# Kernel optimization log

Hardware: AMD Instinct MI355X
Metric: run time of the kernel (lower is better)

## Reference

```python
import jax, jax.numpy as jnp
import numpy as np

B, N, G = 16, 6000, 256
T = 200                     # TRAIN_ROIS_PER_IMAGE
RATIO = 0.33                # POSITIVE_ROI_RATIO
POS_NUM = int(T * RATIO)    # 66 positive slots
NEG_SLOTS = T - POS_NUM     # 134 negative slots
BBOX_STD = jnp.asarray([0.1, 0.1, 0.2, 0.2], jnp.float32)
EPS = 1e-8


def _rand_boxes(key, b, n):
    # valid [y1,x1,y2,x2] boxes in [0,1]
    k1, k2 = jax.random.split(key)
    tl = jax.random.uniform(k1, (b, n, 2)) * 0.7
    wh = jax.random.uniform(k2, (b, n, 2)) * 0.25 + 0.02
    return jnp.concatenate([tl, tl + wh], axis=-1).astype(jnp.float32)


def setup_inputs() -> dict:
    key = jax.random.key(0)
    k1, k2, k3, k4, k5 = jax.random.split(key, 5)
    rois = _rand_boxes(k1, B, N)
    rois = rois.at[:, N - 1000:].set(0.0)          # zero padding tail (remove_zero_padding)
    gt_boxes = _rand_boxes(k2, B, G)
    gt_ids = jax.random.randint(k3, (B, G), 1, 81, dtype=jnp.int32)
    gt_ids = gt_ids.at[:, G - 32:G - 16].set(-1)   # crowd boxes (ids < 0)
    gt_ids = gt_ids.at[:, G - 16:].set(0)          # padded gt
    gt_boxes = gt_boxes.at[:, G - 16:].set(0.0)
    pos_score = jax.random.uniform(k4, (B, N), dtype=jnp.float32)
    neg_score = jax.random.uniform(k5, (B, N), dtype=jnp.float32)
    return {"rois": rois, "gt_ids": gt_ids, "gt_boxes": gt_boxes,
            "pos_score": pos_score, "neg_score": neg_score}


def _pairwise_iou(a, b):
    # a:[N,4], b:[G,4] -> [N,G]
    y1 = jnp.maximum(a[:, None, 0], b[None, :, 0])
    x1 = jnp.maximum(a[:, None, 1], b[None, :, 1])
    y2 = jnp.minimum(a[:, None, 2], b[None, :, 2])
    x2 = jnp.minimum(a[:, None, 3], b[None, :, 3])
    inter = jnp.clip(y2 - y1, 0.0) * jnp.clip(x2 - x1, 0.0)
    area_a = (a[:, 2] - a[:, 0]) * (a[:, 3] - a[:, 1])
    area_b = (b[:, 2] - b[:, 0]) * (b[:, 3] - b[:, 1])
    union = area_a[:, None] + area_b[None, :] - inter
    return inter / jnp.maximum(union, EPS)


def _bbox_offset(boxes, gt):
    h = jnp.maximum(boxes[:, 2] - boxes[:, 0], EPS)
    w = jnp.maximum(boxes[:, 3] - boxes[:, 1], EPS)
    cy = boxes[:, 0] + 0.5 * h
    cx = boxes[:, 1] + 0.5 * w
    gh = jnp.maximum(gt[:, 2] - gt[:, 0], EPS)
    gw = jnp.maximum(gt[:, 3] - gt[:, 1], EPS)
    gcy = gt[:, 0] + 0.5 * gh
    gcx = gt[:, 1] + 0.5 * gw
    off = jnp.stack([(gcy - cy) / h, (gcx - cx) / w,
                     jnp.log(gh / h), jnp.log(gw / w)], axis=1)
    return off / BBOX_STD


def _per_image(rois, gt_ids, gt_boxes, pos_score, neg_score):
    roi_valid = jnp.any(rois != 0.0, axis=1)        # [N]
    gt_valid = jnp.any(gt_boxes != 0.0, axis=1)     # [G]
    crowd = gt_valid & (gt_ids < 0)
    non_crowd = gt_valid & (gt_ids > 0)

    iou = _pairwise_iou(rois, gt_boxes)             # [N,G]
    iou_nc = jnp.where(non_crowd[None, :], iou, -1.0)
    iou_nc_max = jnp.max(iou_nc, axis=1)
    iou_cr_max = jnp.max(jnp.where(crowd[None, :], iou, 0.0), axis=1)

    pos_mask = roi_valid & (iou_nc_max >= 0.5)
    neg_mask = roi_valid & (iou_nc_max < 0.5) & (iou_cr_max < 0.001)

    # random sampling == sort by iid uniform scores (masked out -> -inf)
    pos_idx = jnp.argsort(-jnp.where(pos_mask, pos_score, -jnp.inf))[:POS_NUM]
    pos_count = jnp.minimum(jnp.sum(pos_mask), POS_NUM).astype(jnp.int32)
    pos_slot_valid = jnp.arange(POS_NUM) < pos_count

    neg_target = (jnp.float32(1.0 / RATIO) * pos_count.astype(jnp.float32)).astype(jnp.int32) - pos_count
    neg_idx = jnp.argsort(-jnp.where(neg_mask, neg_score, -jnp.inf))[:NEG_SLOTS]
    neg_count = jnp.minimum(jnp.sum(neg_mask).astype(jnp.int32),
                            jnp.minimum(neg_target, NEG_SLOTS))
    neg_slot_valid = jnp.arange(NEG_SLOTS) < neg_count

    pos_rois_raw = rois[pos_idx]                                   # [P,4]
    pos_rois = jnp.where(pos_slot_valid[:, None], pos_rois_raw, 0.0)
    neg_rois = jnp.where(neg_slot_valid[:, None], rois[neg_idx], 0.0)

    assign = jnp.argmax(iou_nc[pos_idx], axis=1)                   # gt assignment
    roi_gt_boxes = gt_boxes[assign]
    roi_gt_ids = jnp.where(pos_slot_valid, gt_ids[assign], 0)

    off = _bbox_offset(pos_rois_raw, roi_gt_boxes)
    off = jnp.where(pos_slot_valid[:, None], off, 0.0)

    out_rois = jnp.concatenate([pos_rois, neg_rois], axis=0)       # [T,4]
    out_ids = jnp.pad(roi_gt_ids, (0, NEG_SLOTS))                  # [T]
    out_off = jnp.pad(off, ((0, NEG_SLOTS), (0, 0)))               # [T,4]
    return out_rois, out_ids, out_off


def reference(rois, gt_ids, gt_boxes, pos_score, neg_score):
    return jax.vmap(_per_image)(rois, gt_ids, gt_boxes, pos_score, neg_score)
```

## Files before the change

kernel.cpp:

```cpp
#include <hip/hip_runtime.h>

#define BIMG 16
#define NROI 6000
#define NGT  256
#define TPOS 66
#define TNEG 134
#define TTOT 200
#define EPSF 1e-8f
#define INVALID_SCORE 0xFFFFFFFFu

typedef unsigned long long u64;
typedef unsigned int u32;
typedef unsigned char u8;

__global__ __launch_bounds__(256)
void iou_keys_kernel(const float* __restrict__ rois,
                     const int* __restrict__ gt_ids,
                     const float* __restrict__ gt_boxes,
                     const float* __restrict__ pos_score,
                     const float* __restrict__ neg_score,
                     u32* __restrict__ pos_s,
                     u32* __restrict__ neg_s,
                     u8* __restrict__ assign)
{
#pragma clang fp contract(off)
    const int b = blockIdx.y;
    __shared__ float4 s_ncbox[NGT];
    __shared__ float2 s_ncai[NGT];
    __shared__ float4 s_crbox[NGT];
    __shared__ float  s_crarea[NGT];
    __shared__ int s_nccnt, s_crcnt;

    if (threadIdx.x == 0) { s_nccnt = 0; s_crcnt = 0; }
    __syncthreads();
    {
        const int g = threadIdx.x;
        float4 gb = ((const float4*)gt_boxes)[b * NGT + g];
        bool valid = (gb.x != 0.f) || (gb.y != 0.f) || (gb.z != 0.f) || (gb.w != 0.f);
        int id = gt_ids[b * NGT + g];
        float area = (gb.z - gb.x) * (gb.w - gb.y);
        if (valid && id > 0) {
            int slot = atomicAdd(&s_nccnt, 1);
            s_ncbox[slot] = gb;
            s_ncai[slot] = make_float2(area, (float)g);
        } else if (valid && id < 0) {
            int slot = atomicAdd(&s_crcnt, 1);
            s_crbox[slot] = gb;
            s_crarea[slot] = area;
        }
    }
    __syncthreads();
    const int nccnt = s_nccnt;
    const int crcnt = s_crcnt;

    const int r_local = threadIdx.x >> 3;
    const int sub = threadIdx.x & 7;
    const int n = blockIdx.x * 32 + r_local;
    const int n_eff = min(n, NROI - 1);

    float4 rb = ((const float4*)rois)[b * NROI + n_eff];
    const bool rvalid = (rb.x != 0.f) || (rb.y != 0.f) || (rb.z != 0.f) || (rb.w != 0.f);
    const float area_a = (rb.z - rb.x) * (rb.w - rb.y);

    float best = -1.0f;
    float bestg = 0.0f;
    float crmax = 0.0f;

    for (int i = sub; i < nccnt; i += 8) {
        float4 p0 = s_ncbox[i];
        float2 ai = s_ncai[i];
        float y1 = fmaxf(rb.x, p0.x);
        float x1 = fmaxf(rb.y, p0.y);
        float y2 = fminf(rb.z, p0.z);
        float x2 = fminf(rb.w, p0.w);
        float ih = fmaxf(y2 - y1, 0.0f);
        float iw = fmaxf(x2 - x1, 0.0f);
        float inter = ih * iw;
        float uni = fmaxf(area_a + ai.x - inter, EPSF);
        float iou = inter / uni;
        bool better = (iou > best) || ((iou == best) && (ai.y < bestg));
        if (better) { best = iou; bestg = ai.y; }
    }
    for (int i = sub; i < crcnt; i += 8) {
        float4 p0 = s_crbox[i];
        float y1 = fmaxf(rb.x, p0.x);
        float x1 = fmaxf(rb.y, p0.y);
        float y2 = fminf(rb.z, p0.z);
        float x2 = fminf(rb.w, p0.w);
        float ih = fmaxf(y2 - y1, 0.0f);
        float iw = fmaxf(x2 - x1, 0.0f);
        float inter = ih * iw;
        float uni = fmaxf(area_a + s_crarea[i] - inter, EPSF);
        crmax = fmaxf(crmax, inter / uni);
    }

    for (int m = 1; m <= 4; m <<= 1) {
        float ov = __shfl_xor(best, m);
        float og = __shfl_xor(bestg, m);
        float oc = __shfl_xor(crmax, m);
        if ((ov > best) || ((ov == best) && (og < bestg))) { best = ov; bestg = og; }
        crmax = fmaxf(crmax, oc);
    }

    if (sub == 0 && n < NROI) {
        u32 ps = INVALID_SCORE, ns = INVALID_SCORE;
        if (rvalid) {
            if (best >= 0.5f)
                ps = __float_as_uint(pos_score[b * NROI + n]);
            if ((best < 0.5f) && (crmax < 0.001f))
                ns = __float_as_uint(neg_score[b * NROI + n]);
        }
        pos_s[b * NROI + n] = ps;
        neg_s[b * NROI + n] = ns;
        assign[b * NROI + n] = (u8)(int)bestg;
    }
}

#define BSEL 512
#define SLOTS 12
#define CAND_CAP 256

struct SelShared {
    u32 hist[2048];
    u32 wtot[8];
    u32 wsuf[8];
    int pick;
    u32 higher;
    u32 pickpop;
    u32 count;
    u64 comp[CAND_CAP];
    int cnt;
    int sel[TNEG];
};

__device__ __forceinline__ int count_valid(const u32* __restrict__ src,
                                           int tid, int lane, SelShared* S)
{
    int myvalid = 0;
    for (int s = 0; s < SLOTS; ++s) {
        int idx = s * BSEL + tid;
        myvalid += (idx < NROI && src[idx] != INVALID_SCORE);
    }
    for (int off = 1; off < 64; off <<= 1) myvalid += __shfl_xor(myvalid, off);
    if (tid == 0) S->count = 0;
    __syncthreads();
    if (lane == 0) atomicAdd(&S->count, (u32)myvalid);
    __syncthreads();
    return (int)S->count;
}

__device__ __forceinline__ int radix_select(const u32* __restrict__ src, int K,
                                            int tid, int lane, int w, SelShared* S)
{
    u32 sc[SLOTS];
    int myvalid = 0;
    for (int s = 0; s < SLOTS; ++s) {
        int idx = s * BSEL + tid;
        sc[s] = (idx < NROI) ? src[idx] : INVALID_SCORE;
        myvalid += (sc[s] != INVALID_SCORE);
    }
    for (int off = 1; off < 64; off <<= 1) myvalid += __shfl_xor(myvalid, off);
    if (tid == 0) S->count = 0;
    __syncthreads();
    if (lane == 0) atomicAdd(&S->count, (u32)myvalid);
    __syncthreads();
    const int total = (int)S->count;
    const int K0 = min(K, total);
    if (K0 <= 0) return total;

    int Krem = K0;
    u64 prefix = 0ull, mask = 0ull;
    int cand = total;

    for (int p = 3; p >= 0; --p) {
        if (cand <= CAND_CAP) break;
        const int shift = p * 11;
        for (int i = tid; i < 2048; i += BSEL) S->hist[i] = 0;
        __syncthreads();
        for (int s = 0; s < SLOTS; ++s) {
            if (sc[s] != INVALID_SCORE) {
                u64 k = ((u64)sc[s] << 13) | (u64)(8191 - (s * BSEL + tid));
                if ((k & mask) == prefix)
                    atomicAdd(&S->hist[(u32)(k >> shift) & 2047u], 1u);
            }
        }
        __syncthreads();
        u32 local = S->hist[4 * tid] + S->hist[4 * tid + 1]
                  + S->hist[4 * tid + 2] + S->hist[4 * tid + 3];
        u32 suf = local;
        for (int off = 1; off < 64; off <<= 1) {
            u32 v = __shfl_down(suf, off);
            if (lane + off < 64) suf += v;
        }
        if (lane == 0) S->wtot[w] = suf;
        __syncthreads();
        if (tid < 8) {
            u32 t = 0;
            for (int j = tid + 1; j < 8; ++j) t += S->wtot[j];
            S->wsuf[tid] = t;
        }
        __syncthreads();
        u32 Sincl = suf + S->wsuf[w];
        for (int k2 = 0; k2 < 4; ++k2) {
            u32 h = S->hist[4 * tid + k2];
            u32 Snext = Sincl - h;
            if (Sincl >= (u32)Krem && Snext < (u32)Krem) {
                S->pick = 4 * tid + k2;
                S->higher = Snext;
                S->pickpop = h;
            }
            Sincl = Snext;
        }
        __syncthreads();
        prefix |= ((u64)(u32)S->pick) << shift;
        mask   |= (2047ull << shift);
        Krem   -= (int)S->higher;
        cand    = (K0 - Krem) + (int)S->pickpop;
        __syncthreads();
    }

    if (tid == 0) S->cnt = 0;
    __syncthreads();
    for (int s = 0; s < SLOTS; ++s) {
        if (sc[s] != INVALID_SCORE) {
            u64 k = ((u64)sc[s] << 13) | (u64)(8191 - (s * BSEL + tid));
            if ((k & mask) >= prefix) {
                int pos = atomicAdd(&S->cnt, 1);
                S->comp[pos] = k;
            }
        }
    }
    __syncthreads();
    const int Cnt = S->cnt;
    if (tid < Cnt) {
        u64 k = S->comp[tid];
        int rank = 0;
        for (int j = 0; j < Cnt; ++j) rank += (S->comp[j] > k);
        if (rank < K0) S->sel[rank] = 8191 - (int)(k & 8191ull);
    }
    __syncthreads();
    return total;
}

__global__ __launch_bounds__(BSEL)
void select_gather_kernel(const float* __restrict__ rois,
                          const int* __restrict__ gt_ids,
                          const float* __restrict__ gt_boxes,
                          const u32* __restrict__ pos_s,
                          const u32* __restrict__ neg_s,
                          const u8* __restrict__ assign,
                          float* __restrict__ out)
{
#pragma clang fp contract(off)
    __shared__ SelShared S;
    const int b = blockIdx.x >> 1;
    const int side = blockIdx.x & 1;
    const int tid = threadIdx.x;
    const int lane = tid & 63;
    const int w = tid >> 6;

    float* out_rois = out;
    float* out_ids  = out + BIMG * TTOT * 4;
    float* out_off  = out + BIMG * TTOT * 4 + BIMG * TTOT;

    if (side == 0) {
        const int pos_total = radix_select(pos_s + (size_t)b * NROI, TPOS,
                                           tid, lane, w, &S);
        const int pos_count = min(pos_total, TPOS);

        if (tid < TPOS) {
            const int base = b * TTOT + tid;
            float4 ro  = make_float4(0.f, 0.f, 0.f, 0.f);
            float  idv = 0.f;
            float4 off = make_float4(0.f, 0.f, 0.f, 0.f);
            if (tid < pos_count) {
                int n = S.sel[tid];
                float4 rb = ((const float4*)rois)[b * NROI + n];
                ro = rb;
                int g = (int)assign[b * NROI + n];
                float4 gb = ((const float4*)gt_boxes)[b * NGT + g];
                idv = (float)gt_ids[b * NGT + g];

                float h  = fmaxf(rb.z - rb.x, EPSF);
                float wd = fmaxf(rb.w - rb.y, EPSF);
                float cy = rb.x + 0.5f * h;
                float cx = rb.y + 0.5f * wd;
                float gh = fmaxf(gb.z - gb.x, EPSF);
                float gw = fmaxf(gb.w - gb.y, EPSF);
                float gcy = gb.x + 0.5f * gh;
                float gcx = gb.y + 0.5f * gw;
                off.x = ((gcy - cy) / h)  / 0.1f;
                off.y = ((gcx - cx) / wd) / 0.1f;
                off.z = logf(gh / h)  / 0.2f;
                off.w = logf(gw / wd) / 0.2f;
            }
            ((float4*)out_rois)[base] = ro;
            out_ids[base] = idv;
            ((float4*)out_off)[base] = off;
        }
    } else {
        const int pos_total = count_valid(pos_s + (size_t)b * NROI, tid, lane, &S);
        const int pos_count = min(pos_total, TPOS);
        const float ratio_inv = (float)(1.0 / 0.33);
        const int neg_target = (int)(ratio_inv * (float)pos_count) - pos_count;

        const int neg_total = radix_select(neg_s + (size_t)b * NROI, TNEG,
                                           tid, lane, w, &S);
        const int neg_count = max(0, min(neg_total, min(neg_target, TNEG)));

        if (tid < TNEG) {
            const int base = b * TTOT + TPOS + tid;
            float4 ro = make_float4(0.f, 0.f, 0.f, 0.f);
            if (tid < neg_count) {
                int n = S.sel[tid];
                ro = ((const float4*)rois)[b * NROI + n];
            }
            ((float4*)out_rois)[base] = ro;
            out_ids[base] = 0.f;
            ((float4*)out_off)[base] = make_float4(0.f, 0.f, 0.f, 0.f);
        }
    }
}

extern "C" void kernel_launch(void* const* d_in, const int* in_sizes, int n_in,
                              void* d_out, int out_size, void* d_ws, size_t ws_size,
                              hipStream_t stream) {
    const float* rois      = (const float*)d_in[0];
    const int*   gt_ids    = (const int*)d_in[1];
    const float* gt_boxes  = (const float*)d_in[2];
    const float* pos_score = (const float*)d_in[3];
    const float* neg_score = (const float*)d_in[4];
    float* out = (float*)d_out;

    char* ws = (char*)d_ws;
    u32* pos_s = (u32*)(ws + 0);
    u32* neg_s = (u32*)(ws + 384000);
    u8*  assign = (u8*)(ws + 768000);

    dim3 gridA((NROI + 31) / 32, BIMG);
    iou_keys_kernel<<<gridA, 256, 0, stream>>>(rois, gt_ids, gt_boxes,
                                               pos_score, neg_score,
                                               pos_s, neg_s, assign);
    select_gather_kernel<<<BIMG * 2, BSEL, 0, stream>>>(rois, gt_ids, gt_boxes,
                                                        pos_s, neg_s, assign, out);
}
```

Baseline: 92.21 us.

## Fuse IoU and selection kernels into one launch with per-image completion counters

Merges the IoU/key kernel and the radix-select/gather kernel into a single launch. Per-image atomic counters are released by phase-1 blocks, and phase-2 blocks spin on them with acquire loads before selecting. Selection blocks shrink to 256 threads and now re-read scores from global memory on each radix pass instead of holding them in registers. This removes one kernel launch boundary and lets selection start per image as soon as that image is ready. It adds a memset, spin-wait risk if blocks are not scheduled in order, and extra global reads.

```diff
diff --git a/kernel.cpp b/kernel.cpp
--- a/kernel.cpp
+++ b/kernel.cpp
@@ -9,29 +9,50 @@
 #define EPSF 1e-8f
 #define INVALID_SCORE 0xFFFFFFFFu
 
+#define UNITS 188
+#define P1_BLOCKS (UNITS * BIMG)
+#define NT 256
+#define SLOTS 24
+#define CAND_CAP 384
+
 typedef unsigned long long u64;
 typedef unsigned int u32;
 typedef unsigned char u8;
 
-__global__ __launch_bounds__(256)
-void iou_keys_kernel(const float* __restrict__ rois,
-                     const int* __restrict__ gt_ids,
-                     const float* __restrict__ gt_boxes,
-                     const float* __restrict__ pos_score,
-                     const float* __restrict__ neg_score,
-                     u32* __restrict__ pos_s,
-                     u32* __restrict__ neg_s,
-                     u8* __restrict__ assign)
+struct P1Shared {
+    float4 ncbox[NGT];
+    float2 ncai[NGT];
+    float4 crbox[NGT];
+    float  crarea[NGT];
+    int nccnt, crcnt;
+};
+
+struct SelShared {
+    u32 hist[2048];
+    u32 wtot[4];
+    u32 wsuf[4];
+    int pick;
+    u32 higher;
+    u32 pickpop;
+    u32 count;
+    u64 comp[CAND_CAP];
+    int cnt;
+    int sel[TNEG];
+};
+
+__device__ __forceinline__ void phase1_block(
+    int unit,
+    const float* __restrict__ rois, const int* __restrict__ gt_ids,
+    const float* __restrict__ gt_boxes, const float* __restrict__ pos_score,
+    const float* __restrict__ neg_score, u32* __restrict__ pos_s,
+    u32* __restrict__ neg_s, u8* __restrict__ assign, u32* __restrict__ ctr,
+    P1Shared& S)
 {
 #pragma clang fp contract(off)
-    const int b = blockIdx.y;
-    __shared__ float4 s_ncbox[NGT];
-    __shared__ float2 s_ncai[NGT];
-    __shared__ float4 s_crbox[NGT];
-    __shared__ float  s_crarea[NGT];
-    __shared__ int s_nccnt, s_crcnt;
-
-    if (threadIdx.x == 0) { s_nccnt = 0; s_crcnt = 0; }
+    const int b = unit / UNITS;
+    const int c = unit - b * UNITS;
+
+    if (threadIdx.x == 0) { S.nccnt = 0; S.crcnt = 0; }
     __syncthreads();
     {
         const int g = threadIdx.x;
@@ -40,22 +61,22 @@
         int id = gt_ids[b * NGT + g];
         float area = (gb.z - gb.x) * (gb.w - gb.y);
         if (valid && id > 0) {
-            int slot = atomicAdd(&s_nccnt, 1);
-            s_ncbox[slot] = gb;
-            s_ncai[slot] = make_float2(area, (float)g);
+            int slot = atomicAdd(&S.nccnt, 1);
+            S.ncbox[slot] = gb;
+            S.ncai[slot] = make_float2(area, (float)g);
         } else if (valid && id < 0) {
-            int slot = atomicAdd(&s_crcnt, 1);
-            s_crbox[slot] = gb;
-            s_crarea[slot] = area;
-        }
-    }
-    __syncthreads();
-    const int nccnt = s_nccnt;
-    const int crcnt = s_crcnt;
+            int slot = atomicAdd(&S.crcnt, 1);
+            S.crbox[slot] = gb;
+            S.crarea[slot] = area;
+        }
+    }
+    __syncthreads();
+    const int nccnt = S.nccnt;
+    const int crcnt = S.crcnt;
 
     const int r_local = threadIdx.x >> 3;
     const int sub = threadIdx.x & 7;
-    const int n = blockIdx.x * 32 + r_local;
+    const int n = c * 32 + r_local;
     const int n_eff = min(n, NROI - 1);
 
     float4 rb = ((const float4*)rois)[b * NROI + n_eff];
@@ -67,8 +88,8 @@
     float crmax = 0.0f;
 
     for (int i = sub; i < nccnt; i += 8) {
-        float4 p0 = s_ncbox[i];
-        float2 ai = s_ncai[i];
+        float4 p0 = S.ncbox[i];
+        float2 ai = S.ncai[i];
         float y1 = fmaxf(rb.x, p0.x);
         float x1 = fmaxf(rb.y, p0.y);
         float y2 = fminf(rb.z, p0.z);
@@ -82,7 +103,7 @@
         if (better) { best = iou; bestg = ai.y; }
     }
     for (int i = sub; i < crcnt; i += 8) {
-        float4 p0 = s_crbox[i];
+        float4 p0 = S.crbox[i];
         float y1 = fmaxf(rb.x, p0.x);
         float x1 = fmaxf(rb.y, p0.y);
         float y2 = fminf(rb.z, p0.z);
@@ -90,7 +111,7 @@
         float ih = fmaxf(y2 - y1, 0.0f);
         float iw = fmaxf(x2 - x1, 0.0f);
         float inter = ih * iw;
-        float uni = fmaxf(area_a + s_crarea[i] - inter, EPSF);
+        float uni = fmaxf(area_a + S.crarea[i] - inter, EPSF);
         crmax = fmaxf(crmax, inter / uni);
     }
 
@@ -114,31 +135,18 @@
         neg_s[b * NROI + n] = ns;
         assign[b * NROI + n] = (u8)(int)bestg;
     }
-}
-
-#define BSEL 512
-#define SLOTS 12
-#define CAND_CAP 256
-
-struct SelShared {
-    u32 hist[2048];
-    u32 wtot[8];
-    u32 wsuf[8];
-    int pick;
-    u32 higher;
-    u32 pickpop;
-    u32 count;
-    u64 comp[CAND_CAP];
-    int cnt;
-    int sel[TNEG];
-};
+
+    __syncthreads();
+    if (threadIdx.x == 0)
+        __hip_atomic_fetch_add(&ctr[b], 1u, __ATOMIC_RELEASE, __HIP_MEMORY_SCOPE_AGENT);
+}
 
 __device__ __forceinline__ int count_valid(const u32* __restrict__ src,
                                            int tid, int lane, SelShared* S)
 {
     int myvalid = 0;
     for (int s = 0; s < SLOTS; ++s) {
-        int idx = s * BSEL + tid;
+        int idx = s * NT + tid;
         myvalid += (idx < NROI && src[idx] != INVALID_SCORE);
     }
     for (int off = 1; off < 64; off <<= 1) myvalid += __shfl_xor(myvalid, off);
@@ -146,18 +154,18 @@
     __syncthreads();
     if (lane == 0) atomicAdd(&S->count, (u32)myvalid);
     __syncthreads();
-    return (int)S->count;
+    int tot = (int)S->count;
+    __syncthreads();
+    return tot;
 }
 
 __device__ __forceinline__ int radix_select(const u32* __restrict__ src, int K,
                                             int tid, int lane, int w, SelShared* S)
 {
-    u32 sc[SLOTS];
     int myvalid = 0;
     for (int s = 0; s < SLOTS; ++s) {
-        int idx = s * BSEL + tid;
-        sc[s] = (idx < NROI) ? src[idx] : INVALID_SCORE;
-        myvalid += (sc[s] != INVALID_SCORE);
+        int idx = s * NT + tid;
+        myvalid += (idx < NROI && src[idx] != INVALID_SCORE);
     }
     for (int off = 1; off < 64; off <<= 1) myvalid += __shfl_xor(myvalid, off);
     if (tid == 0) S->count = 0;
@@ -175,18 +183,23 @@
     for (int p = 3; p >= 0; --p) {
         if (cand <= CAND_CAP) break;
         const int shift = p * 11;
-        for (int i = tid; i < 2048; i += BSEL) S->hist[i] = 0;
+        for (int i = tid; i < 2048; i += NT) S->hist[i] = 0;
         __syncthreads();
         for (int s = 0; s < SLOTS; ++s) {
-            if (sc[s] != INVALID_SCORE) {
-                u64 k = ((u64)sc[s] << 13) | (u64)(8191 - (s * BSEL + tid));
-                if ((k & mask) == prefix)
-                    atomicAdd(&S->hist[(u32)(k >> shift) & 2047u], 1u);
-            }
-        }
-        __syncthreads();
-        u32 local = S->hist[4 * tid] + S->hist[4 * tid + 1]
-                  + S->hist[4 * tid + 2] + S->hist[4 * tid + 3];
+            int idx = s * NT + tid;
+            if (idx < NROI) {
+                u32 v = src[idx];
+                if (v != INVALID_SCORE) {
+                    u64 k = ((u64)v << 13) | (u64)(8191 - idx);
+                    if ((k & mask) == prefix)
+                        atomicAdd(&S->hist[(u32)(k >> shift) & 2047u], 1u);
+                }
+            }
+        }
+        __syncthreads();
+        u32 local = 0;
+#pragma unroll
+        for (int j = 0; j < 8; ++j) local += S->hist[8 * tid + j];
         u32 suf = local;
         for (int off = 1; off < 64; off <<= 1) {
             u32 v = __shfl_down(suf, off);
@@ -194,18 +207,18 @@
         }
         if (lane == 0) S->wtot[w] = suf;
         __syncthreads();
-        if (tid < 8) {
+        if (tid < 4) {
             u32 t = 0;
-            for (int j = tid + 1; j < 8; ++j) t += S->wtot[j];
+            for (int j = tid + 1; j < 4; ++j) t += S->wtot[j];
             S->wsuf[tid] = t;
         }
         __syncthreads();
         u32 Sincl = suf + S->wsuf[w];
-        for (int k2 = 0; k2 < 4; ++k2) {
-            u32 h = S->hist[4 * tid + k2];
+        for (int k2 = 0; k2 < 8; ++k2) {
+            u32 h = S->hist[8 * tid + k2];
             u32 Snext = Sincl - h;
             if (Sincl >= (u32)Krem && Snext < (u32)Krem) {
-                S->pick = 4 * tid + k2;
+                S->pick = 8 * tid + k2;
                 S->higher = Snext;
                 S->pickpop = h;
             }
@@ -222,18 +235,22 @@
     if (tid == 0) S->cnt = 0;
     __syncthreads();
     for (int s = 0; s < SLOTS; ++s) {
-        if (sc[s] != INVALID_SCORE) {
-            u64 k = ((u64)sc[s] << 13) | (u64)(8191 - (s * BSEL + tid));
-            if ((k & mask) >= prefix) {
-                int pos = atomicAdd(&S->cnt, 1);
-                S->comp[pos] = k;
+        int idx = s * NT + tid;
+        if (idx < NROI) {
+            u32 v = src[idx];
+            if (v != INVALID_SCORE) {
+                u64 k = ((u64)v << 13) | (u64)(8191 - idx);
+                if ((k & mask) >= prefix) {
+                    int pos = atomicAdd(&S->cnt, 1);
+                    S->comp[pos] = k;
+                }
             }
         }
     }
     __syncthreads();
     const int Cnt = S->cnt;
-    if (tid < Cnt) {
-        u64 k = S->comp[tid];
+    for (int c0 = tid; c0 < Cnt; c0 += NT) {
+        u64 k = S->comp[c0];
         int rank = 0;
         for (int j = 0; j < Cnt; ++j) rank += (S->comp[j] > k);
         if (rank < K0) S->sel[rank] = 8191 - (int)(k & 8191ull);
@@ -242,22 +259,26 @@
     return total;
 }
 
-__global__ __launch_bounds__(BSEL)
-void select_gather_kernel(const float* __restrict__ rois,
-                          const int* __restrict__ gt_ids,
-                          const float* __restrict__ gt_boxes,
-                          const u32* __restrict__ pos_s,
-                          const u32* __restrict__ neg_s,
-                          const u8* __restrict__ assign,
-                          float* __restrict__ out)
+__device__ __forceinline__ void phase2_block(
+    int wbid,
+    const float* __restrict__ rois, const int* __restrict__ gt_ids,
+    const float* __restrict__ gt_boxes, const u32* __restrict__ pos_s,
+    const u32* __restrict__ neg_s, const u8* __restrict__ assign,
+    u32* __restrict__ ctr, float* __restrict__ out, SelShared& S)
 {
 #pragma clang fp contract(off)
-    __shared__ SelShared S;
-    const int b = blockIdx.x >> 1;
-    const int side = blockIdx.x & 1;
+    const int b = wbid >> 1;
+    const int side = wbid & 1;
     const int tid = threadIdx.x;
     const int lane = tid & 63;
     const int w = tid >> 6;
+
+    if (tid == 0) {
+        while (__hip_atomic_load(&ctr[b], __ATOMIC_ACQUIRE,
+                                 __HIP_MEMORY_SCOPE_AGENT) < (u32)UNITS)
+            __builtin_amdgcn_s_sleep(8);
+    }
+    __syncthreads();
 
     float* out_rois = out;
     float* out_ids  = out + BIMG * TTOT * 4;
@@ -322,6 +343,33 @@
     }
 }
 
+__global__ __launch_bounds__(NT, 8)
+void fused_kernel(const float* __restrict__ rois,
+                  const int* __restrict__ gt_ids,
+                  const float* __restrict__ gt_boxes,
+                  const float* __restrict__ pos_score,
+                  const float* __restrict__ neg_score,
+                  u32* __restrict__ pos_s,
+                  u32* __restrict__ neg_s,
+                  u8* __restrict__ assign,
+                  u32* __restrict__ ctr,
+                  float* __restrict__ out)
+{
+    constexpr size_t SB = sizeof(P1Shared) > sizeof(SelShared)
+                        ? sizeof(P1Shared) : sizeof(SelShared);
+    __shared__ __align__(16) char smem[SB];
+
+    if (blockIdx.x < P1_BLOCKS) {
+        phase1_block((int)blockIdx.x, rois, gt_ids, gt_boxes, pos_score,
+                     neg_score, pos_s, neg_s, assign, ctr,
+                     *reinterpret_cast<P1Shared*>(smem));
+    } else {
+        phase2_block((int)blockIdx.x - P1_BLOCKS, rois, gt_ids, gt_boxes,
+                     pos_s, neg_s, assign, ctr, out,
+                     *reinterpret_cast<SelShared*>(smem));
+    }
+}
+
 extern "C" void kernel_launch(void* const* d_in, const int* in_sizes, int n_in,
                               void* d_out, int out_size, void* d_ws, size_t ws_size,
                               hipStream_t stream) {
@@ -336,11 +384,11 @@
     u32* pos_s = (u32*)(ws + 0);
     u32* neg_s = (u32*)(ws + 384000);
     u8*  assign = (u8*)(ws + 768000);
-
-    dim3 gridA((NROI + 31) / 32, BIMG);
-    iou_keys_kernel<<<gridA, 256, 0, stream>>>(rois, gt_ids, gt_boxes,
-                                               pos_score, neg_score,
-                                               pos_s, neg_s, assign);
-    select_gather_kernel<<<BIMG * 2, BSEL, 0, stream>>>(rois, gt_ids, gt_boxes,
-                                                        pos_s, neg_s, assign, out);
-}
+    u32* ctr    = (u32*)(ws + 864000);
+
+    hipMemsetAsync(ctr, 0, BIMG * sizeof(u32), stream);
+
+    fused_kernel<<<P1_BLOCKS + 2 * BIMG, NT, 0, stream>>>(
+        rois, gt_ids, gt_boxes, pos_score, neg_score,
+        pos_s, neg_s, assign, ctr, out);
+}
```

After: 166.5 us. 1.81x slower.
